# Kernel tuning notes

Hardware: AMD Instinct MI355X
Metric: run time of the kernel (lower is better)

The kernel has to match this reference:

```python
import jax, jax.numpy as jnp
import numpy as np

B, T, D, E = 4, 1024, 1024, 8
HD = 4 * D  # hdim = 4*dim


def setup_inputs() -> dict:
    key = jax.random.key(0)
    k1, k2, k3, k4 = jax.random.split(key, 4)
    std = 0.5 * D ** (-0.5)
    bound = (3.0 ** 0.5) * std
    x = jax.random.normal(k1, (B, T, D), dtype=jnp.float32)
    # router zero-init in source; use small random weights so routing is non-degenerate
    router_w = jax.random.normal(k2, (E, D), dtype=jnp.float32) * 0.02
    expert_fc = jax.random.uniform(k3, (E, D, HD), dtype=jnp.float32, minval=-bound, maxval=bound)
    # proj zero-init in source; use small random so output/backward are non-trivial
    expert_proj = jax.random.normal(k4, (E, D, HD), dtype=jnp.float32) * 0.02
    return {"x": x, "router_w": router_w, "expert_fc": expert_fc, "expert_proj": expert_proj}


def reference(x, router_w, expert_fc, expert_proj):
    # router: Linear(dim, E, bias=False) -> logits [B,T,E]
    logits = jnp.einsum('btd,ed->bte', x, router_w)
    probs = jax.nn.softmax(logits, axis=-1)
    expert_ids = jnp.argmax(probs, axis=-1)  # [B,T]; top-1 (max) routing
    # NOTE: source computes expert_weights (max prob) but does NOT use it in combine.
    mask = jax.nn.one_hot(expert_ids, E, dtype=x.dtype)  # [B,T,E]
    # Dense all-experts compute (faithful to source): h = x @ fc (F.linear with fc.T)
    h = jnp.einsum('btd,edh->ebth', x, expert_fc)
    h = jnp.square(jax.nn.relu(h))  # relu(h)**2
    # expert_output = h @ proj.T (F.linear with proj [dim, hdim])
    out_e = jnp.einsum('ebth,edh->ebtd', h, expert_proj)
    # masked combine: sum_e out_e * (ids == e)
    output = jnp.einsum('ebtd,bte->btd', out_e, mask)
    return output
```

## Files before the change

kernel.cpp:

```cpp
#include <hip/hip_runtime.h>
#include <hip/hip_bf16.h>
#include <stdint.h>

#define NE 8
#define DIM 1024
#define HDIM 4096
#define NTOK 4096
#define KSPLIT 4
#define MAXT 40

typedef unsigned short ushort_t;
typedef __attribute__((ext_vector_type(4))) float f32x4;
typedef __attribute__((ext_vector_type(8))) short bf16x8;

__device__ __forceinline__ ushort_t f2b(float f) {
  union { float f; unsigned u; } c; c.f = f;
  unsigned u = c.u;
  return (ushort_t)((u + 0x7fffu + ((u >> 16) & 1u)) >> 16);
}

__device__ __forceinline__ void gl2lds16(const void* g, void* l) {
  __builtin_amdgcn_global_load_lds(
      (__attribute__((address_space(1))) void*)g,
      (__attribute__((address_space(3))) void*)l, 16, 0, 0);
}

__global__ __launch_bounds__(256) void router_kernel(
    const float* __restrict__ x, const float* __restrict__ rw,
    int* __restrict__ eid, int* __restrict__ rank, int* __restrict__ cnt) {
  __shared__ float w[NE * 1028];
  for (int i = threadIdx.x; i < NE * DIM; i += 256) {
    int e = i >> 10, d = i & 1023;
    w[e * 1028 + d] = rw[i];
  }
  __syncthreads();
  int grp = threadIdx.x >> 3;
  int e = threadIdx.x & 7;
  int t = blockIdx.x * 32 + grp;
  const float4* xr = (const float4*)(x + (size_t)t * DIM);
  const float4* wr = (const float4*)(w + e * 1028);
  float acc = 0.f;
#pragma unroll 4
  for (int i = 0; i < DIM / 4; ++i) {
    float4 xv = xr[i], wv = wr[i];
    acc += xv.x * wv.x + xv.y * wv.y + xv.z * wv.z + xv.w * wv.w;
  }
  float v = acc; int ie = e;
#pragma unroll
  for (int m = 4; m; m >>= 1) {
    float ov = __shfl_xor(v, m, 8);
    int oi = __shfl_xor(ie, m, 8);
    if (ov > v || (ov == v && oi < ie)) { v = ov; ie = oi; }
  }
  if (e == 0) {
    eid[t] = ie;
    rank[t] = atomicAdd(&cnt[ie], 1);
  }
}

__global__ void scan_kernel(const int* __restrict__ cnt, int* __restrict__ offs,
                            int* __restrict__ tile_e, int* __restrict__ tile_m,
                            int* __restrict__ ntiles) {
  if (threadIdx.x == 0) {
    int s = 0, nt = 0;
    for (int e = 0; e < NE; ++e) {
      offs[e] = s;
      int c = cnt[e];
      for (int m = 0; m < c; m += 128) { tile_e[nt] = e; tile_m[nt] = m; ++nt; }
      s += c;
    }
    offs[NE] = s;
    *ntiles = nt;
  }
}

__global__ __launch_bounds__(256) void gather_kernel(
    const float* __restrict__ x, const int* __restrict__ eid,
    const int* __restrict__ rank, const int* __restrict__ offs,
    int* __restrict__ sorted, ushort_t* __restrict__ Xg) {
  int t = blockIdx.x;
  int e = eid[t];
  int pos = offs[e] + rank[t];
  if (threadIdx.x == 0) sorted[pos] = t;
  int i = threadIdx.x;
  float4 v = ((const float4*)(x + (size_t)t * DIM))[i];
  ushort4 o = make_ushort4(f2b(v.x), f2b(v.y), f2b(v.z), f2b(v.w));
  *(ushort4*)(Xg + (size_t)pos * DIM + i * 4) = o;
}

__global__ __launch_bounds__(256) void transpose_fc_kernel(
    const float* __restrict__ fc, ushort_t* __restrict__ fct) {
  __shared__ float tile[32][33];
  int e = blockIdx.z;
  int h0 = blockIdx.x * 32, d0 = blockIdx.y * 32;
  int c = threadIdx.x & 31, r0 = threadIdx.x >> 5;
  const float* src = fc + ((size_t)e * DIM + d0) * HDIM + h0 + c;
#pragma unroll
  for (int i = 0; i < 4; ++i) {
    int r = r0 + i * 8;
    tile[r][c] = src[(size_t)r * HDIM];
  }
  __syncthreads();
  ushort_t* dst = fct + ((size_t)e * HDIM + h0) * DIM + d0 + c;
#pragma unroll
  for (int i = 0; i < 4; ++i) {
    int r = r0 + i * 8;
    dst[(size_t)r * DIM] = f2b(tile[c][r]);
  }
}

__global__ __launch_bounds__(256) void convert_kernel(
    const float* __restrict__ p, ushort_t* __restrict__ o) {
  size_t i = (size_t)blockIdx.x * 256 + threadIdx.x;
  float4 v = ((const float4*)p)[i];
  ushort4 u = make_ushort4(f2b(v.x), f2b(v.y), f2b(v.z), f2b(v.w));
  ((ushort4*)o)[i] = u;
}

__global__ __launch_bounds__(256, 2) void gemm1_kernel(
    const ushort_t* __restrict__ Xg, const ushort_t* __restrict__ fct,
    const int* __restrict__ offs, const int* __restrict__ tile_e,
    const int* __restrict__ tile_m, const int* __restrict__ ntiles,
    ushort_t* __restrict__ H) {
  if ((int)blockIdx.y >= *ntiles) return;
  int e = tile_e[blockIdx.y];
  int mb = tile_m[blockIdx.y];
  int m0 = offs[e];
  int Me = offs[e + 1] - m0;
  int n0 = blockIdx.x * 128;

  __shared__ ushort_t As[128 * 32];
  __shared__ ushort_t Bs[128 * 32];

  int tid = threadIdx.x;
  int wave = tid >> 6;
  int lane = tid & 63;

  const ushort_t* ap[2]; const ushort_t* bp[2];
  ushort_t* al[2]; ushort_t* bl[2];
#pragma unroll
  for (int q = 0; q < 2; ++q) {
    int rl = (wave * 2 + q) * 16 + (lane >> 2);
    int kc = (lane & 3) * 8;
    int rg = mb + rl; if (rg >= Me) rg = Me - 1;
    ap[q] = Xg + (size_t)(m0 + rg) * DIM + kc;
    bp[q] = fct + ((size_t)e * HDIM + n0 + rl) * DIM + kc;
    al[q] = &As[(wave * 2 + q) * 512];
    bl[q] = &Bs[(wave * 2 + q) * 512];
  }

  f32x4 acc[4][4] = {};
  int wm = (wave & 1) * 64;
  int wn = (wave >> 1) * 64;
  int fr = lane & 15;
  int kq = (lane >> 4) * 8;

  for (int k0 = 0; k0 < DIM; k0 += 32) {
    gl2lds16(ap[0] + k0, al[0]);
    gl2lds16(ap[1] + k0, al[1]);
    gl2lds16(bp[0] + k0, bl[0]);
    gl2lds16(bp[1] + k0, bl[1]);
    __syncthreads();
    bf16x8 af[4], bf[4];
#pragma unroll
    for (int i = 0; i < 4; ++i) {
      af[i] = *(const bf16x8*)&As[(wm + i * 16 + fr) * 32 + kq];
      bf[i] = *(const bf16x8*)&Bs[(wn + i * 16 + fr) * 32 + kq];
    }
#pragma unroll
    for (int i = 0; i < 4; ++i)
#pragma unroll
      for (int j = 0; j < 4; ++j)
        acc[i][j] = __builtin_amdgcn_mfma_f32_16x16x32_bf16(af[i], bf[j], acc[i][j], 0, 0, 0);
    __syncthreads();
  }

  int cq = (lane >> 4) * 4;
#pragma unroll
  for (int i = 0; i < 4; ++i) {
#pragma unroll
    for (int r = 0; r < 4; ++r) {
      int rl = wm + i * 16 + cq + r;
      int rg = mb + rl;
      if (rg < Me) {
        ushort_t* dst = H + (size_t)(m0 + rg) * HDIM + n0 + wn + (lane & 15);
#pragma unroll
        for (int j = 0; j < 4; ++j) {
          float v = acc[i][j][r];
          v = fmaxf(v, 0.f);
          dst[j * 16] = f2b(v * v);
        }
      }
    }
  }
}

__global__ __launch_bounds__(256, 2) void gemm2_kernel(
    const ushort_t* __restrict__ Hm, const ushort_t* __restrict__ pjb,
    const int* __restrict__ offs, const int* __restrict__ tile_e,
    const int* __restrict__ tile_m, const int* __restrict__ ntiles,
    const int* __restrict__ sorted, float* __restrict__ out) {
  if ((int)blockIdx.y >= *ntiles) return;
  int e = tile_e[blockIdx.y];
  int mb = tile_m[blockIdx.y];
  int ks = blockIdx.z;
  int m0 = offs[e];
  int Me = offs[e + 1] - m0;
  int n0 = blockIdx.x * 128;

  __shared__ ushort_t As[128 * 32];
  __shared__ ushort_t Bs[128 * 32];

  int tid = threadIdx.x;
  int wave = tid >> 6;
  int lane = tid & 63;

  const ushort_t* ap[2]; const ushort_t* bp[2];
  ushort_t* al[2]; ushort_t* bl[2];
#pragma unroll
  for (int q = 0; q < 2; ++q) {
    int rl = (wave * 2 + q) * 16 + (lane >> 2);
    int kc = (lane & 3) * 8;
    int rg = mb + rl; if (rg >= Me) rg = Me - 1;
    ap[q] = Hm + (size_t)(m0 + rg) * HDIM + kc;
    bp[q] = pjb + ((size_t)e * DIM + n0 + rl) * HDIM + kc;
    al[q] = &As[(wave * 2 + q) * 512];
    bl[q] = &Bs[(wave * 2 + q) * 512];
  }

  f32x4 acc[4][4] = {};
  int wm = (wave & 1) * 64;
  int wn = (wave >> 1) * 64;
  int fr = lane & 15;
  int kq = (lane >> 4) * 8;

  int kbeg = ks * (HDIM / KSPLIT);
  int kend = kbeg + (HDIM / KSPLIT);
  for (int k0 = kbeg; k0 < kend; k0 += 32) {
    gl2lds16(ap[0] + k0, al[0]);
    gl2lds16(ap[1] + k0, al[1]);
    gl2lds16(bp[0] + k0, bl[0]);
    gl2lds16(bp[1] + k0, bl[1]);
    __syncthreads();
    bf16x8 af[4], bf[4];
#pragma unroll
    for (int i = 0; i < 4; ++i) {
      af[i] = *(const bf16x8*)&As[(wm + i * 16 + fr) * 32 + kq];
      bf[i] = *(const bf16x8*)&Bs[(wn + i * 16 + fr) * 32 + kq];
    }
#pragma unroll
    for (int i = 0; i < 4; ++i)
#pragma unroll
      for (int j = 0; j < 4; ++j)
        acc[i][j] = __builtin_amdgcn_mfma_f32_16x16x32_bf16(af[i], bf[j], acc[i][j], 0, 0, 0);
    __syncthreads();
  }

  int cq = (lane >> 4) * 4;
#pragma unroll
  for (int i = 0; i < 4; ++i) {
#pragma unroll
    for (int r = 0; r < 4; ++r) {
      int rl = wm + i * 16 + cq + r;
      int rg = mb + rl;
      if (rg < Me) {
        int tok = sorted[m0 + rg];
        float* dst = out + (size_t)tok * DIM + n0 + wn + (lane & 15);
#pragma unroll
        for (int j = 0; j < 4; ++j) atomicAdd(dst + j * 16, acc[i][j][r]);
      }
    }
  }
}

extern "C" void kernel_launch(void* const* d_in, const int* in_sizes, int n_in,
                              void* d_out, int out_size, void* d_ws, size_t ws_size,
                              hipStream_t stream) {
  const float* x  = (const float*)d_in[0];
  const float* rw = (const float*)d_in[1];
  const float* fc = (const float*)d_in[2];
  const float* pj = (const float*)d_in[3];
  float* out = (float*)d_out;
  char* ws = (char*)d_ws;

  int* eid        = (int*)(ws + 0x0000);
  int* rank       = (int*)(ws + 0x4000);
  int* cnt        = (int*)(ws + 0x8000);
  int* offs       = (int*)(ws + 0x8100);
  int* tile_e     = (int*)(ws + 0x8200);
  int* tile_m     = (int*)(ws + 0x8600);
  int* ntiles     = (int*)(ws + 0x8a00);
  int* sorted     = (int*)(ws + 0x9000);
  ushort_t* Xg    = (ushort_t*)(ws + 0x10000);
  ushort_t* H     = (ushort_t*)(ws + 0x810000);
  ushort_t* W     = (ushort_t*)(ws + 0x2810000);

  hipMemsetAsync(cnt, 0, 32, stream);
  hipMemsetAsync(out, 0, (size_t)out_size * sizeof(float), stream);
  router_kernel<<<NTOK / 32, 256, 0, stream>>>(x, rw, eid, rank, cnt);
  scan_kernel<<<1, 64, 0, stream>>>(cnt, offs, tile_e, tile_m, ntiles);
  gather_kernel<<<NTOK, 256, 0, stream>>>(x, eid, rank, offs, sorted, Xg);
  transpose_fc_kernel<<<dim3(HDIM / 32, DIM / 32, NE), 256, 0, stream>>>(fc, W);
  gemm1_kernel<<<dim3(HDIM / 128, MAXT), 256, 0, stream>>>(Xg, W, offs, tile_e, tile_m, ntiles, H);
  convert_kernel<<<(NE * DIM * HDIM / 4) / 256, 256, 0, stream>>>(pj, W);
  gemm2_kernel<<<dim3(DIM / 128, MAXT, KSPLIT), 256, 0, stream>>>(H, W, offs, tile_e, tile_m, ntiles, sorted, out);
}
```

Baseline: 522.8 us.

## Fuse proj fp32-to-bf16 conversion into gemm2 and replace atomics with split-K reduce

```diff
diff --git a/kernel.cpp b/kernel.cpp
--- a/kernel.cpp
+++ b/kernel.cpp
@@ -17,6 +17,18 @@
   union { float f; unsigned u; } c; c.f = f;
   unsigned u = c.u;
   return (ushort_t)((u + 0x7fffu + ((u >> 16) & 1u)) >> 16);
+}
+
+__device__ __forceinline__ bf16x8 cvt8(const float* p) {
+  f32x4 lo = *(const f32x4*)p;
+  f32x4 hi = *(const f32x4*)(p + 4);
+  union { unsigned u[4]; bf16x8 v; } r;
+  union { float f; unsigned u; } a, b;
+  a.f = lo[0]; b.f = lo[1]; r.u[0] = __builtin_amdgcn_perm(b.u, a.u, 0x07060302);
+  a.f = lo[2]; b.f = lo[3]; r.u[1] = __builtin_amdgcn_perm(b.u, a.u, 0x07060302);
+  a.f = hi[0]; b.f = hi[1]; r.u[2] = __builtin_amdgcn_perm(b.u, a.u, 0x07060302);
+  a.f = hi[2]; b.f = hi[3]; r.u[3] = __builtin_amdgcn_perm(b.u, a.u, 0x07060302);
+  return r.v;
 }
 
 __device__ __forceinline__ void gl2lds16(const void* g, void* l) {
@@ -109,14 +121,6 @@
   }
 }
 
-__global__ __launch_bounds__(256) void convert_kernel(
-    const float* __restrict__ p, ushort_t* __restrict__ o) {
-  size_t i = (size_t)blockIdx.x * 256 + threadIdx.x;
-  float4 v = ((const float4*)p)[i];
-  ushort4 u = make_ushort4(f2b(v.x), f2b(v.y), f2b(v.z), f2b(v.w));
-  ((ushort4*)o)[i] = u;
-}
-
 __global__ __launch_bounds__(256, 2) void gemm1_kernel(
     const ushort_t* __restrict__ Xg, const ushort_t* __restrict__ fct,
     const int* __restrict__ offs, const int* __restrict__ tile_e,
@@ -196,10 +200,10 @@
 }
 
 __global__ __launch_bounds__(256, 2) void gemm2_kernel(
-    const ushort_t* __restrict__ Hm, const ushort_t* __restrict__ pjb,
+    const ushort_t* __restrict__ Hm, const float* __restrict__ pj,
     const int* __restrict__ offs, const int* __restrict__ tile_e,
     const int* __restrict__ tile_m, const int* __restrict__ ntiles,
-    const int* __restrict__ sorted, float* __restrict__ out) {
+    float* __restrict__ P) {
   if ((int)blockIdx.y >= *ntiles) return;
   int e = tile_e[blockIdx.y];
   int mb = tile_m[blockIdx.y];
@@ -209,23 +213,29 @@
   int n0 = blockIdx.x * 128;
 
   __shared__ ushort_t As[128 * 32];
-  __shared__ ushort_t Bs[128 * 32];
+  __shared__ float Bs[128 * 36];
 
   int tid = threadIdx.x;
   int wave = tid >> 6;
   int lane = tid & 63;
 
-  const ushort_t* ap[2]; const ushort_t* bp[2];
-  ushort_t* al[2]; ushort_t* bl[2];
+  const ushort_t* ap[2]; ushort_t* al[2];
 #pragma unroll
   for (int q = 0; q < 2; ++q) {
     int rl = (wave * 2 + q) * 16 + (lane >> 2);
     int kc = (lane & 3) * 8;
     int rg = mb + rl; if (rg >= Me) rg = Me - 1;
     ap[q] = Hm + (size_t)(m0 + rg) * HDIM + kc;
-    bp[q] = pjb + ((size_t)e * DIM + n0 + rl) * HDIM + kc;
     al[q] = &As[(wave * 2 + q) * 512];
-    bl[q] = &Bs[(wave * 2 + q) * 512];
+  }
+
+  const float* bsrc[4]; float* bdst[4];
+#pragma unroll
+  for (int p = 0; p < 4; ++p) {
+    int row = p * 32 + (tid >> 3);
+    int ch = tid & 7;
+    bsrc[p] = pj + ((size_t)e * DIM + n0 + row) * HDIM + ch * 4;
+    bdst[p] = &Bs[row * 36 + ch * 4];
   }
 
   f32x4 acc[4][4] = {};
@@ -239,14 +249,17 @@
   for (int k0 = kbeg; k0 < kend; k0 += 32) {
     gl2lds16(ap[0] + k0, al[0]);
     gl2lds16(ap[1] + k0, al[1]);
-    gl2lds16(bp[0] + k0, bl[0]);
-    gl2lds16(bp[1] + k0, bl[1]);
+    float4 bv[4];
+#pragma unroll
+    for (int p = 0; p < 4; ++p) bv[p] = *(const float4*)(bsrc[p] + k0);
+#pragma unroll
+    for (int p = 0; p < 4; ++p) *(float4*)bdst[p] = bv[p];
     __syncthreads();
     bf16x8 af[4], bf[4];
 #pragma unroll
     for (int i = 0; i < 4; ++i) {
       af[i] = *(const bf16x8*)&As[(wm + i * 16 + fr) * 32 + kq];
-      bf[i] = *(const bf16x8*)&Bs[(wn + i * 16 + fr) * 32 + kq];
+      bf[i] = cvt8(&Bs[(wn + i * 16 + fr) * 36 + kq]);
     }
 #pragma unroll
     for (int i = 0; i < 4; ++i)
@@ -264,13 +277,25 @@
       int rl = wm + i * 16 + cq + r;
       int rg = mb + rl;
       if (rg < Me) {
-        int tok = sorted[m0 + rg];
-        float* dst = out + (size_t)tok * DIM + n0 + wn + (lane & 15);
-#pragma unroll
-        for (int j = 0; j < 4; ++j) atomicAdd(dst + j * 16, acc[i][j][r]);
+        float* dst = P + ((size_t)ks * NTOK + (m0 + rg)) * DIM + n0 + wn + (lane & 15);
+#pragma unroll
+        for (int j = 0; j < 4; ++j) dst[j * 16] = acc[i][j][r];
       }
     }
   }
+}
+
+__global__ __launch_bounds__(256) void reduce_kernel(
+    const float* __restrict__ P, const int* __restrict__ sorted,
+    float* __restrict__ out) {
+  int pos = blockIdx.x;
+  int tok = sorted[pos];
+  int i = threadIdx.x;
+  size_t base = (size_t)pos * DIM + i * 4;
+  const size_t S = (size_t)NTOK * DIM;
+  f32x4 s = *(const f32x4*)(P + base) + *(const f32x4*)(P + S + base) +
+            *(const f32x4*)(P + 2 * S + base) + *(const f32x4*)(P + 3 * S + base);
+  *(f32x4*)(out + (size_t)tok * DIM + i * 4) = s;
 }
 
 extern "C" void kernel_launch(void* const* d_in, const int* in_sizes, int n_in,
@@ -294,14 +319,14 @@
   ushort_t* Xg    = (ushort_t*)(ws + 0x10000);
   ushort_t* H     = (ushort_t*)(ws + 0x810000);
   ushort_t* W     = (ushort_t*)(ws + 0x2810000);
+  float* P        = (float*)W;
 
   hipMemsetAsync(cnt, 0, 32, stream);
-  hipMemsetAsync(out, 0, (size_t)out_size * sizeof(float), stream);
   router_kernel<<<NTOK / 32, 256, 0, stream>>>(x, rw, eid, rank, cnt);
   scan_kernel<<<1, 64, 0, stream>>>(cnt, offs, tile_e, tile_m, ntiles);
   gather_kernel<<<NTOK, 256, 0, stream>>>(x, eid, rank, offs, sorted, Xg);
   transpose_fc_kernel<<<dim3(HDIM / 32, DIM / 32, NE), 256, 0, stream>>>(fc, W);
   gemm1_kernel<<<dim3(HDIM / 128, MAXT), 256, 0, stream>>>(Xg, W, offs, tile_e, tile_m, ntiles, H);
-  convert_kernel<<<(NE * DIM * HDIM / 4) / 256, 256, 0, stream>>>(pj, W);
-  gemm2_kernel<<<dim3(DIM / 128, MAXT, KSPLIT), 256, 0, stream>>>(H, W, offs, tile_e, tile_m, ntiles, sorted, out);
-}
+  gemm2_kernel<<<dim3(DIM / 128, MAXT, KSPLIT), 256, 0, stream>>>(H, pj, offs, tile_e, tile_m, ntiles, P);
+  reduce_kernel<<<NTOK, 256, 0, stream>>>(P, sorted, out);
+}
```

After: 492.2 us. 1.06x faster.
